# Kernel tuning notes

Hardware: AMD Instinct MI355X
Metric: run time of the kernel (lower is better)

## Reference

```python
import jax, jax.numpy as jnp
import numpy as np

NUM_GRAPHS = 128
NODES_PER_GRAPH = 512
NUM_NODES = NUM_GRAPHS * NODES_PER_GRAPH
NUM_EDGES = NUM_NODES * 16
IN_DIM = 64
HID = 128
NUM_HEADS = 4
BN_EPS = 1e-5


def setup_inputs() -> dict:
    key = jax.random.key(0)
    ks = jax.random.split(key, 12)
    x = jax.random.normal(ks[0], (NUM_NODES, IN_DIM), dtype=jnp.float32)
    edge_index = jax.random.randint(ks[1], (2, NUM_EDGES), 0, NUM_NODES, dtype=jnp.int32)
    batch = jnp.repeat(jnp.arange(NUM_GRAPHS, dtype=jnp.int32), NODES_PER_GRAPH)
    s = 0.05
    W0 = jax.random.normal(ks[2], (IN_DIM, HID), dtype=jnp.float32) * s
    b0 = jnp.zeros((HID,), jnp.float32)
    Wh = jax.random.normal(ks[3], (3, HID, HID), dtype=jnp.float32) * s  # convs 1..3
    bh = jnp.zeros((3, HID), jnp.float32)
    bn_gamma = jnp.ones((4, HID), jnp.float32)
    bn_beta = jnp.zeros((4, HID), jnp.float32)
    bn_mean = jnp.zeros((4, HID), jnp.float32)
    bn_var = jnp.ones((4, HID), jnp.float32)
    attn_in_w = jax.random.normal(ks[4], (3 * HID, HID), dtype=jnp.float32) * s
    attn_in_b = jnp.zeros((3 * HID,), jnp.float32)
    attn_out_w = jax.random.normal(ks[5], (HID, HID), dtype=jnp.float32) * s
    attn_out_b = jnp.zeros((HID,), jnp.float32)
    return dict(x=x, W0=W0, b0=b0, Wh=Wh, bh=bh, bn_gamma=bn_gamma, bn_beta=bn_beta,
                bn_mean=bn_mean, bn_var=bn_var, attn_in_w=attn_in_w, attn_in_b=attn_in_b,
                attn_out_w=attn_out_w, attn_out_b=attn_out_b, edge_index=edge_index, batch=batch)


def _forward(x, W0, b0, Wh, bh, bn_gamma, bn_beta, bn_mean, bn_var,
             attn_in_w, attn_in_b, attn_out_w, attn_out_b, edge_index, batch):
    N = x.shape[0]
    src, dst = edge_index[0], edge_index[1]
    # GCN symmetric normalization with self-loops (PyG GCNConv)
    deg = jax.ops.segment_sum(jnp.ones_like(src, jnp.float32), dst, num_segments=N) + 1.0
    dis = jax.lax.rsqrt(deg)                      # deg^{-1/2}
    enorm = (dis[src] * dis[dst])[:, None]        # per-edge norm
    self_norm = (dis * dis)[:, None]              # self-loop norm

    def gcn(h, W, b):
        h = h @ W
        agg = jax.ops.segment_sum(h[src] * enorm, dst, num_segments=N)
        return agg + h * self_norm + b

    def bn(h, i):
        scale = bn_gamma[i] * jax.lax.rsqrt(bn_var[i] + BN_EPS)
        return (h - bn_mean[i]) * scale + bn_beta[i]  # eval-mode BN

    # dropout is identity in eval mode
    h = jax.nn.relu(bn(gcn(x, W0, b0), 0))
    h = jax.nn.relu(bn(gcn(h, Wh[0], bh[0]), 1))
    h = jax.nn.relu(bn(gcn(h, Wh[1], bh[1]), 2))
    f = jax.nn.relu(bn(gcn(h, Wh[2], bh[2]), 3))   # [N, HID]

    # per-graph self-attention (equal-size contiguous graphs -> batched MHA)
    dh = HID // NUM_HEADS
    xg = f.reshape(NUM_GRAPHS, NODES_PER_GRAPH, HID)
    qkv = xg @ attn_in_w.T + attn_in_b            # [G, n, 3H]
    q, k, v = jnp.split(qkv, 3, axis=-1)

    def heads(t):
        return t.reshape(NUM_GRAPHS, NODES_PER_GRAPH, NUM_HEADS, dh).transpose(0, 2, 1, 3)
    q, k, v = heads(q), heads(k), heads(v)
    scores = jnp.einsum('ghnd,ghmd->ghnm', q, k) / np.sqrt(dh).astype(np.float32)
    attn = jax.nn.softmax(scores, axis=-1)
    o = jnp.einsum('ghnm,ghmd->ghnd', attn, v).transpose(0, 2, 1, 3).reshape(NUM_GRAPHS, NODES_PER_GRAPH, HID)
    o = o @ attn_out_w.T + attn_out_b
    final = o.reshape(N, HID)

    # global mean pool over batch indices
    cnt = jax.ops.segment_sum(jnp.ones((N,), jnp.float32), batch, num_segments=NUM_GRAPHS)
    graph_emb = jax.ops.segment_sum(final, batch, num_segments=NUM_GRAPHS) / cnt[:, None]
    return final, graph_emb


def reference(x, W0, b0, Wh, bh, bn_gamma, bn_beta, bn_mean, bn_var,
              attn_in_w, attn_in_b, attn_out_w, attn_out_b, edge_index, batch):
    return _forward(x, W0, b0, Wh, bh, bn_gamma, bn_beta, bn_mean, bn_var,
                    attn_in_w, attn_in_b, attn_out_w, attn_out_b, edge_index, batch)
```

## Files before the change

kernel.cpp:

```cpp
#include <hip/hip_runtime.h>
#include <hip/hip_bf16.h>
#include <cstdint>
#include <cstddef>

#define N_NODES 65536
#define N_EDGES 1048576
#define N_GRAPHS 128
#define NPG 512
#define IN_DIM 64
#define HID 128
#define BN_EPS 1e-5f

typedef __attribute__((ext_vector_type(8))) short bf16x8;
typedef __attribute__((ext_vector_type(4))) float f32x4;
typedef __attribute__((ext_vector_type(8))) unsigned short u16x8;

__device__ inline unsigned short f2bf(float f) {
  unsigned u = __builtin_bit_cast(unsigned, f);
  u = u + 0x7fffu + ((u >> 16) & 1u);
  return (unsigned short)(u >> 16);
}
__device__ inline float bf2f(unsigned short h) {
  unsigned u = ((unsigned)h) << 16;
  return __builtin_bit_cast(float, u);
}
__device__ inline void split_bf(float v, unsigned short& hi, unsigned short& lo) {
  hi = f2bf(v);
  lo = f2bf(v - bf2f(hi));
}

__global__ __launch_bounds__(256) void hist_kernel(const int* __restrict__ dst,
                                                   int* __restrict__ deg) {
  int e = blockIdx.x * 256 + threadIdx.x;
  if (e < N_EDGES) atomicAdd(&deg[dst[e]], 1);
}

__global__ __launch_bounds__(256) void dis_kernel(const int* __restrict__ deg,
                                                  float* __restrict__ dis) {
  int n = blockIdx.x * 256 + threadIdx.x;
  if (n < N_NODES) dis[n] = 1.0f / sqrtf((float)deg[n] + 1.0f);
}

__global__ __launch_bounds__(1024) void scan_kernel(const int* __restrict__ deg,
                                                    int* __restrict__ offsets,
                                                    int* __restrict__ cursor) {
  __shared__ int sums[1024];
  int t = threadIdx.x;
  int base = t * 64;
  const int4* dp = (const int4*)(deg + base);
  int s = 0;
#pragma unroll
  for (int i = 0; i < 16; i++) {
    int4 v = dp[i];
    s += v.x + v.y + v.z + v.w;
  }
  sums[t] = s;
  __syncthreads();
  for (int off = 1; off < 1024; off <<= 1) {
    int v = (t >= off) ? sums[t - off] : 0;
    __syncthreads();
    sums[t] += v;
    __syncthreads();
  }
  int run = (t == 0) ? 0 : sums[t - 1];
#pragma unroll
  for (int i = 0; i < 16; i++) {
    int4 v = dp[i];
    int idx = base + i * 4;
    offsets[idx] = run; cursor[idx] = run; run += v.x;
    offsets[idx + 1] = run; cursor[idx + 1] = run; run += v.y;
    offsets[idx + 2] = run; cursor[idx + 2] = run; run += v.z;
    offsets[idx + 3] = run; cursor[idx + 3] = run; run += v.w;
  }
  if (t == 1023) offsets[N_NODES] = run;
}

__global__ __launch_bounds__(256) void fill_kernel(const int* __restrict__ src,
                                                   const int* __restrict__ dst,
                                                   int* __restrict__ cursor,
                                                   int* __restrict__ csr) {
  int e = blockIdx.x * 256 + threadIdx.x;
  if (e < N_EDGES) {
    int d = dst[e];
    int slot = atomicAdd(&cursor[d], 1);
    csr[slot] = src[e];
  }
}

__global__ __launch_bounds__(256) void agg64_kernel(const float* __restrict__ x,
                                                    const float* __restrict__ dis,
                                                    const int* __restrict__ offsets,
                                                    const int* __restrict__ csr,
                                                    unsigned short* __restrict__ zhi,
                                                    unsigned short* __restrict__ zlo) {
  int node = blockIdx.x * 4 + (threadIdx.x >> 6);
  int lane = threadIdx.x & 63;
  float dn = dis[node];
  float acc = x[(size_t)node * 64 + lane] * dn * dn;
  int beg = offsets[node], end = offsets[node + 1];
  int k = beg;
  for (; k + 4 <= end; k += 4) {
    int s0 = csr[k], s1 = csr[k + 1], s2 = csr[k + 2], s3 = csr[k + 3];
    float w0 = dn * dis[s0], w1 = dn * dis[s1], w2 = dn * dis[s2], w3 = dn * dis[s3];
    float v0 = x[(size_t)s0 * 64 + lane];
    float v1 = x[(size_t)s1 * 64 + lane];
    float v2 = x[(size_t)s2 * 64 + lane];
    float v3 = x[(size_t)s3 * 64 + lane];
    acc = fmaf(w0, v0, acc);
    acc = fmaf(w1, v1, acc);
    acc = fmaf(w2, v2, acc);
    acc = fmaf(w3, v3, acc);
  }
  for (; k < end; k++) {
    int s = csr[k];
    acc = fmaf(dn * dis[s], x[(size_t)s * 64 + lane], acc);
  }
  unsigned short h_, l_;
  split_bf(acc, h_, l_);
  zhi[(size_t)node * 64 + lane] = h_;
  zlo[(size_t)node * 64 + lane] = l_;
}

__global__ __launch_bounds__(256) void agg128_kernel(const float* __restrict__ h,
                                                     const float* __restrict__ dis,
                                                     const int* __restrict__ offsets,
                                                     const int* __restrict__ csr,
                                                     unsigned short* __restrict__ zhi,
                                                     unsigned short* __restrict__ zlo) {
  int node = blockIdx.x * 4 + (threadIdx.x >> 6);
  int lane = threadIdx.x & 63;
  float dn = dis[node];
  float sn = dn * dn;
  const float* hr = h + (size_t)node * 128;
  float a0 = hr[lane] * sn;
  float a1 = hr[lane + 64] * sn;
  int beg = offsets[node], end = offsets[node + 1];
  int k = beg;
  for (; k + 4 <= end; k += 4) {
    int s0 = csr[k], s1 = csr[k + 1], s2 = csr[k + 2], s3 = csr[k + 3];
    float w0 = dn * dis[s0], w1 = dn * dis[s1], w2 = dn * dis[s2], w3 = dn * dis[s3];
    const float* p0 = h + (size_t)s0 * 128;
    const float* p1 = h + (size_t)s1 * 128;
    const float* p2 = h + (size_t)s2 * 128;
    const float* p3 = h + (size_t)s3 * 128;
    float u0 = p0[lane], d0 = p0[lane + 64];
    float u1 = p1[lane], d1 = p1[lane + 64];
    float u2 = p2[lane], d2 = p2[lane + 64];
    float u3 = p3[lane], d3 = p3[lane + 64];
    a0 = fmaf(w0, u0, a0); a1 = fmaf(w0, d0, a1);
    a0 = fmaf(w1, u1, a0); a1 = fmaf(w1, d1, a1);
    a0 = fmaf(w2, u2, a0); a1 = fmaf(w2, d2, a1);
    a0 = fmaf(w3, u3, a0); a1 = fmaf(w3, d3, a1);
  }
  for (; k < end; k++) {
    int s = csr[k];
    float w = dn * dis[s];
    const float* hs = h + (size_t)s * 128;
    a0 = fmaf(w, hs[lane], a0);
    a1 = fmaf(w, hs[lane + 64], a1);
  }
  unsigned short h0, l0, h1, l1;
  split_bf(a0, h0, l0);
  split_bf(a1, h1, l1);
  zhi[(size_t)node * 128 + lane] = h0;
  zlo[(size_t)node * 128 + lane] = l0;
  zhi[(size_t)node * 128 + lane + 64] = h1;
  zlo[(size_t)node * 128 + lane + 64] = l1;
}

template <bool TRANS>
__global__ __launch_bounds__(256) void wprep_kernel(const float* __restrict__ W, int K, int O,
                                                    unsigned short* __restrict__ hi,
                                                    unsigned short* __restrict__ lo) {
  int idx = blockIdx.x * 256 + threadIdx.x;
  int KC = K / 32;
  int total = (O / 16) * KC * 64;
  if (idx >= total) return;
  int lane = idx & 63;
  int rest = idx >> 6;
  int kc = rest % KC;
  int nt = rest / KC;
  int n = nt * 16 + (lane & 15);
  int kb = kc * 32 + (lane >> 4) * 8;
  unsigned short* hp = hi + (size_t)idx * 8;
  unsigned short* lp = lo + (size_t)idx * 8;
#pragma unroll
  for (int j = 0; j < 8; j++) {
    int k = kb + j;
    float v = TRANS ? W[(size_t)n * K + k] : W[(size_t)k * O + n];
    unsigned short h_, l_;
    split_bf(v, h_, l_);
    hp[j] = h_;
    lp[j] = l_;
  }
}

template <int K, int O, bool DOBN, bool DORELU, bool SPLIT_OUT>
__global__ __launch_bounds__(256) void gemm_mfma(
    const unsigned short* __restrict__ Ahi, const unsigned short* __restrict__ Alo,
    const unsigned short* __restrict__ Whi, const unsigned short* __restrict__ Wlo,
    const float* __restrict__ bias,
    const float* __restrict__ gamma, const float* __restrict__ beta,
    const float* __restrict__ mean, const float* __restrict__ var,
    float* __restrict__ Cf, unsigned short* __restrict__ Chi,
    unsigned short* __restrict__ Clo) {
  constexpr int KC = K / 32;
  int wave = threadIdx.x >> 6;
  int lane = threadIdx.x & 63;
  int m0 = blockIdx.x * 128 + wave * 32;
  int o0 = blockIdx.y * 128;
  int mrow = lane & 15;
  int kseg = (lane >> 4) * 8;

  f32x4 acc[2][8];
#pragma unroll
  for (int mt = 0; mt < 2; mt++)
#pragma unroll
    for (int nt = 0; nt < 8; nt++) acc[mt][nt] = (f32x4)0.0f;

#pragma unroll
  for (int kc = 0; kc < KC; kc++) {
    bf16x8 ah[2], al[2];
#pragma unroll
    for (int mt = 0; mt < 2; mt++) {
      size_t aoff = (size_t)(m0 + mt * 16 + mrow) * K + kc * 32 + kseg;
      ah[mt] = *(const bf16x8*)(Ahi + aoff);
      al[mt] = *(const bf16x8*)(Alo + aoff);
    }
#pragma unroll
    for (int nt = 0; nt < 8; nt++) {
      size_t foff = (((size_t)(blockIdx.y * 8 + nt) * KC + kc) * 64 + lane) * 8;
      bf16x8 bh = *(const bf16x8*)(Whi + foff);
      bf16x8 bl = *(const bf16x8*)(Wlo + foff);
#pragma unroll
      for (int mt = 0; mt < 2; mt++) {
        acc[mt][nt] = __builtin_amdgcn_mfma_f32_16x16x32_bf16(ah[mt], bh, acc[mt][nt], 0, 0, 0);
        acc[mt][nt] = __builtin_amdgcn_mfma_f32_16x16x32_bf16(ah[mt], bl, acc[mt][nt], 0, 0, 0);
        acc[mt][nt] = __builtin_amdgcn_mfma_f32_16x16x32_bf16(al[mt], bh, acc[mt][nt], 0, 0, 0);
        acc[mt][nt] = __builtin_amdgcn_mfma_f32_16x16x32_bf16(al[mt], bl, acc[mt][nt], 0, 0, 0);
      }
    }
  }

  int ccol = lane & 15;
  int crow0 = (lane >> 4) * 4;
#pragma unroll
  for (int nt = 0; nt < 8; nt++) {
    int c = o0 + nt * 16 + ccol;
    float sc, cb;
    float b = bias[c];
    if (DOBN) {
      sc = gamma[c] * rsqrtf(var[c] + BN_EPS);
      cb = (b - mean[c]) * sc + beta[c];
    } else {
      sc = 1.0f;
      cb = b;
    }
#pragma unroll
    for (int mt = 0; mt < 2; mt++) {
#pragma unroll
      for (int r = 0; r < 4; r++) {
        float v = fmaf(acc[mt][nt][r], sc, cb);
        if (DORELU) v = fmaxf(v, 0.0f);
        size_t row = (size_t)(m0 + mt * 16 + crow0 + r);
        if (SPLIT_OUT) {
          unsigned short h_, l_;
          split_bf(v, h_, l_);
          Chi[row * O + c] = h_;
          Clo[row * O + c] = l_;
        } else {
          Cf[row * O + c] = v;
        }
      }
    }
  }
}

__global__ __launch_bounds__(256) void knorm_kernel(const float* __restrict__ qkv,
                                                    float* __restrict__ kmax2) {
  int g = blockIdx.x >> 2;
  int h = blockIdx.x & 3;
  size_t gbase = (size_t)g * NPG;
  float best = 0.0f;
#pragma unroll
  for (int r = 0; r < 2; r++) {
    int j = r * 256 + threadIdx.x;
    const float* kp = &qkv[(gbase + j) * 384 + 128 + h * 32];
    float s = 0.0f;
#pragma unroll
    for (int i = 0; i < 8; i++) {
      float4 v = *(const float4*)(kp + i * 4);
      s = fmaf(v.x, v.x, s);
      s = fmaf(v.y, v.y, s);
      s = fmaf(v.z, v.z, s);
      s = fmaf(v.w, v.w, s);
    }
    best = fmaxf(best, s);
  }
#pragma unroll
  for (int off = 32; off >= 1; off >>= 1)
    best = fmaxf(best, __shfl_xor(best, off, 64));
  __shared__ float red[4];
  int wave = threadIdx.x >> 6;
  if ((threadIdx.x & 63) == 0) red[wave] = best;
  __syncthreads();
  if (threadIdx.x == 0) {
    float m = fmaxf(fmaxf(red[0], red[1]), fmaxf(red[2], red[3]));
    kmax2[blockIdx.x] = m;
  }
}

__global__ __launch_bounds__(256, 2) void attn_mfma_kernel(
    const float* __restrict__ qkv, const float* __restrict__ kmax2,
    unsigned short* __restrict__ ohi, unsigned short* __restrict__ olo) {
  int b = blockIdx.x;
  int g = b >> 3;
  int h = (b >> 1) & 3;
  int half = b & 1;
  int t = threadIdx.x;
  int wave = t >> 6;
  int lane = t & 63;
  int quad = lane >> 4;
  int l15 = lane & 15;
  size_t gbase = (size_t)g * NPG;
  int qb = half * 256 + wave * 64;

  const float cf = 0.17677669529663687f * 1.4426950408889634f;

  __shared__ unsigned short Kh[32][40], Kl[32][40];
  __shared__ unsigned short Vh[33][40], Vl[33][40];
  __shared__ char wbuf[4][10240] __attribute__((aligned(16)));

  unsigned short* Ph = (unsigned short*)wbuf[wave];
  unsigned short* Pl = Ph + 64 * 40;
  float* Ot = (float*)wbuf[wave];

  bf16x8 qh[4], ql[4];
  float qn2p[4];
#pragma unroll
  for (int mt = 0; mt < 4; mt++) {
    const float* qp = &qkv[(gbase + qb + mt * 16 + l15) * 384 + h * 32 + quad * 8];
    float4 f0 = *(const float4*)qp;
    float4 f1 = *(const float4*)(qp + 4);
    float v[8] = {f0.x * cf, f0.y * cf, f0.z * cf, f0.w * cf,
                  f1.x * cf, f1.y * cf, f1.z * cf, f1.w * cf};
    u16x8 hh, ll;
    float s = 0.0f;
#pragma unroll
    for (int j = 0; j < 8; j++) {
      unsigned short hi_, lo_;
      split_bf(v[j], hi_, lo_);
      hh[j] = hi_;
      ll[j] = lo_;
      s = fmaf(v[j], v[j], s);
    }
    qh[mt] = __builtin_bit_cast(bf16x8, hh);
    ql[mt] = __builtin_bit_cast(bf16x8, ll);
    s += __shfl_xor(s, 16);
    s += __shfl_xor(s, 32);
    qn2p[mt] = s;
  }
  if (quad == 0) {
#pragma unroll
    for (int mt = 0; mt < 4; mt++) Ot[mt * 16 + l15] = qn2p[mt];
  }
  float km2 = kmax2[g * 4 + h];
  float Mq[4][4];
#pragma unroll
  for (int mt = 0; mt < 4; mt++)
#pragma unroll
    for (int r = 0; r < 4; r++)
      Mq[mt][r] = sqrtf(Ot[mt * 16 + quad * 4 + r] * km2);

  f32x4 Oa[4][3];
#pragma unroll
  for (int mt = 0; mt < 4; mt++)
#pragma unroll
    for (int nt = 0; nt < 3; nt++) Oa[mt][nt] = (f32x4)0.0f;

  for (int c = 0; c < 16; c++) {
    __syncthreads();
    if (t >= 128) {
      int t2 = t - 128;
      int key = t2 >> 2;
      int ds = (t2 & 3) * 8;
      const float* kp = &qkv[(gbase + (size_t)(c * 32 + key)) * 384 + 128 + h * 32 + ds];
      float4 f0 = *(const float4*)kp;
      float4 f1 = *(const float4*)(kp + 4);
      float v[8] = {f0.x, f0.y, f0.z, f0.w, f1.x, f1.y, f1.z, f1.w};
      u16x8 hh, ll;
#pragma unroll
      for (int j = 0; j < 8; j++) {
        unsigned short hi_, lo_;
        split_bf(v[j], hi_, lo_);
        hh[j] = hi_;
        ll[j] = lo_;
      }
      *(u16x8*)&Kh[key][ds] = hh;
      *(u16x8*)&Kl[key][ds] = ll;
    } else if (t < 64) {
      int keyb = (t & 7) * 4;
      int dvb = (t >> 3) * 4;
      float4 r0 = *(const float4*)&qkv[(gbase + (size_t)(c * 32 + keyb + 0)) * 384 + 256 + h * 32 + dvb];
      float4 r1 = *(const float4*)&qkv[(gbase + (size_t)(c * 32 + keyb + 1)) * 384 + 256 + h * 32 + dvb];
      float4 r2 = *(const float4*)&qkv[(gbase + (size_t)(c * 32 + keyb + 2)) * 384 + 256 + h * 32 + dvb];
      float4 r3 = *(const float4*)&qkv[(gbase + (size_t)(c * 32 + keyb + 3)) * 384 + 256 + h * 32 + dvb];
      float rr[4][4] = {{r0.x, r0.y, r0.z, r0.w}, {r1.x, r1.y, r1.z, r1.w},
                        {r2.x, r2.y, r2.z, r2.w}, {r3.x, r3.y, r3.z, r3.w}};
#pragma unroll
      for (int c2 = 0; c2 < 4; c2++) {
        ushort4 hv, lv;
        unsigned short hi_, lo_;
        split_bf(rr[0][c2], hi_, lo_); hv.x = hi_; lv.x = lo_;
        split_bf(rr[1][c2], hi_, lo_); hv.y = hi_; lv.y = lo_;
        split_bf(rr[2][c2], hi_, lo_); hv.z = hi_; lv.z = lo_;
        split_bf(rr[3][c2], hi_, lo_); hv.w = hi_; lv.w = lo_;
        *(ushort4*)&Vh[dvb + c2][keyb] = hv;
        *(ushort4*)&Vl[dvb + c2][keyb] = lv;
      }
    } else if (t < 68) {
      int i = t - 64;
      u16x8 ones;
#pragma unroll
      for (int j = 0; j < 8; j++) ones[j] = 0x3F80;
      *(u16x8*)&Vh[32][i * 8] = ones;
    }
    __syncthreads();

#pragma unroll
    for (int nt = 0; nt < 2; nt++) {
      bf16x8 bkh = *(const bf16x8*)&Kh[nt * 16 + l15][quad * 8];
      bf16x8 bkl = *(const bf16x8*)&Kl[nt * 16 + l15][quad * 8];
#pragma unroll
      for (int mt = 0; mt < 4; mt++) {
        f32x4 S = (f32x4)0.0f;
        S = __builtin_amdgcn_mfma_f32_16x16x32_bf16(qh[mt], bkh, S, 0, 0, 0);
        S = __builtin_amdgcn_mfma_f32_16x16x32_bf16(qh[mt], bkl, S, 0, 0, 0);
        S = __builtin_amdgcn_mfma_f32_16x16x32_bf16(ql[mt], bkh, S, 0, 0, 0);
        S = __builtin_amdgcn_mfma_f32_16x16x32_bf16(ql[mt], bkl, S, 0, 0, 0);
#pragma unroll
        for (int r = 0; r < 4; r++) {
          float p = __builtin_exp2f(S[r] - Mq[mt][r]);
          unsigned short hi_, lo_;
          split_bf(p, hi_, lo_);
          int row = mt * 16 + quad * 4 + r;
          Ph[row * 40 + nt * 16 + l15] = hi_;
          Pl[row * 40 + nt * 16 + l15] = lo_;
        }
      }
    }
    bf16x8 pah[4], pal[4];
#pragma unroll
    for (int mt = 0; mt < 4; mt++) {
      pah[mt] = *(const bf16x8*)&Ph[(mt * 16 + l15) * 40 + quad * 8];
      pal[mt] = *(const bf16x8*)&Pl[(mt * 16 + l15) * 40 + quad * 8];
    }
#pragma unroll
    for (int nt = 0; nt < 3; nt++) {
      bf16x8 bvh = *(const bf16x8*)&Vh[nt * 16 + l15][quad * 8];
      if (nt < 2) {
        bf16x8 bvl = *(const bf16x8*)&Vl[nt * 16 + l15][quad * 8];
#pragma unroll
        for (int mt = 0; mt < 4; mt++) {
          Oa[mt][nt] = __builtin_amdgcn_mfma_f32_16x16x32_bf16(pah[mt], bvh, Oa[mt][nt], 0, 0, 0);
          Oa[mt][nt] = __builtin_amdgcn_mfma_f32_16x16x32_bf16(pah[mt], bvl, Oa[mt][nt], 0, 0, 0);
          Oa[mt][nt] = __builtin_amdgcn_mfma_f32_16x16x32_bf16(pal[mt], bvh, Oa[mt][nt], 0, 0, 0);
        }
      } else {
#pragma unroll
        for (int mt = 0; mt < 4; mt++) {
          Oa[mt][nt] = __builtin_amdgcn_mfma_f32_16x16x32_bf16(pah[mt], bvh, Oa[mt][nt], 0, 0, 0);
          Oa[mt][nt] = __builtin_amdgcn_mfma_f32_16x16x32_bf16(pal[mt], bvh, Oa[mt][nt], 0, 0, 0);
        }
      }
    }
  }

#pragma unroll
  for (int mt = 0; mt < 4; mt++) {
#pragma unroll
    for (int r = 0; r < 4; r++) {
      int row = mt * 16 + quad * 4 + r;
      Ot[row * 36 + l15] = Oa[mt][0][r];
      Ot[row * 36 + 16 + l15] = Oa[mt][1][r];
      if (l15 == 0) Ot[row * 36 + 32] = Oa[mt][2][r];
    }
  }
  {
    int row = lane;
    float inv = 1.0f / Ot[row * 36 + 32];
    size_t node = gbase + qb + row;
    u16x8 vh, vl;
#pragma unroll
    for (int seg = 0; seg < 4; seg++) {
#pragma unroll
      for (int j = 0; j < 8; j++) {
        unsigned short hi_, lo_;
        split_bf(Ot[row * 36 + seg * 8 + j] * inv, hi_, lo_);
        vh[j] = hi_;
        vl[j] = lo_;
      }
      *(u16x8*)(ohi + node * 128 + h * 32 + seg * 8) = vh;
      *(u16x8*)(olo + node * 128 + h * 32 + seg * 8) = vl;
    }
  }
}

__global__ __launch_bounds__(128) void pool_kernel(const float* __restrict__ fin,
                                                   float* __restrict__ emb) {
  int g = blockIdx.x, c = threadIdx.x;
  const float* p = fin + (size_t)g * NPG * HID + c;
  float s = 0.0f;
  for (int i = 0; i < NPG; i++) s += p[(size_t)i * HID];
  emb[g * HID + c] = s * (1.0f / NPG);
}

extern "C" void kernel_launch(void* const* d_in, const int* in_sizes, int n_in,
                              void* d_out, int out_size, void* d_ws, size_t ws_size,
                              hipStream_t stream) {
  (void)in_sizes; (void)n_in; (void)out_size; (void)ws_size;
  const float* x          = (const float*)d_in[0];
  const float* W0         = (const float*)d_in[1];
  const float* b0         = (const float*)d_in[2];
  const float* Wh         = (const float*)d_in[3];
  const float* bh         = (const float*)d_in[4];
  const float* bn_gamma   = (const float*)d_in[5];
  const float* bn_beta    = (const float*)d_in[6];
  const float* bn_mean    = (const float*)d_in[7];
  const float* bn_var     = (const float*)d_in[8];
  const float* attn_in_w  = (const float*)d_in[9];
  const float* attn_in_b  = (const float*)d_in[10];
  const float* attn_out_w = (const float*)d_in[11];
  const float* attn_out_b = (const float*)d_in[12];
  const int* edge_index   = (const int*)d_in[13];
  const int* src = edge_index;
  const int* dst = edge_index + N_EDGES;

  char* ws = (char*)d_ws;
  size_t off = 0;
  auto alloc = [&](size_t bytes) -> void* {
    void* p = ws + off;
    off += (bytes + 255) & ~(size_t)255;
    return p;
  };
  int*   deg     = (int*)alloc((size_t)N_NODES * 4);
  int*   offsets = (int*)alloc((size_t)(N_NODES + 1) * 4);
  int*   cursor  = (int*)alloc((size_t)N_NODES * 4);
  int*   csr     = (int*)alloc((size_t)N_EDGES * 4);
  float* dis     = (float*)alloc((size_t)N_NODES * 4);
  float* bufA    = (float*)alloc((size_t)N_NODES * HID * 4);
  unsigned short* zhi = (unsigned short*)alloc((size_t)N_NODES * HID * 2);
  unsigned short* zlo = (unsigned short*)alloc((size_t)N_NODES * HID * 2);
  float* qkvb    = (float*)alloc((size_t)N_NODES * 384 * 4);
  float* kmax2   = (float*)alloc((size_t)N_GRAPHS * 4 * 4);
  unsigned short* w0h = (unsigned short*)alloc(8192 * 2);
  unsigned short* w0l = (unsigned short*)alloc(8192 * 2);
  unsigned short* whh[3], *whl[3];
  for (int i = 0; i < 3; i++) {
    whh[i] = (unsigned short*)alloc(16384 * 2);
    whl[i] = (unsigned short*)alloc(16384 * 2);
  }
  unsigned short* wqh = (unsigned short*)alloc(49152 * 2);
  unsigned short* wql = (unsigned short*)alloc(49152 * 2);
  unsigned short* woh = (unsigned short*)alloc(16384 * 2);
  unsigned short* wol = (unsigned short*)alloc(16384 * 2);

  unsigned short* fhi = (unsigned short*)bufA;
  unsigned short* flo = fhi + (size_t)N_NODES * HID;

  float* fin = (float*)d_out;
  float* emb = fin + (size_t)N_NODES * HID;

  hipMemsetAsync(deg, 0, (size_t)N_NODES * 4, stream);
  hist_kernel<<<N_EDGES / 256, 256, 0, stream>>>(dst, deg);
  dis_kernel<<<N_NODES / 256, 256, 0, stream>>>(deg, dis);
  scan_kernel<<<1, 1024, 0, stream>>>(deg, offsets, cursor);
  fill_kernel<<<N_EDGES / 256, 256, 0, stream>>>(src, dst, cursor, csr);

  wprep_kernel<false><<<4, 256, 0, stream>>>(W0, 64, 128, w0h, w0l);
  for (int i = 0; i < 3; i++)
    wprep_kernel<false><<<8, 256, 0, stream>>>(Wh + (size_t)i * HID * HID, 128, 128,
                                               whh[i], whl[i]);
  wprep_kernel<true><<<24, 256, 0, stream>>>(attn_in_w, 128, 384, wqh, wql);
  wprep_kernel<true><<<8, 256, 0, stream>>>(attn_out_w, 128, 128, woh, wol);

  dim3 ggrid(N_NODES / 128, 1);
  agg64_kernel<<<N_NODES / 4, 256, 0, stream>>>(x, dis, offsets, csr, zhi, zlo);
  gemm_mfma<64, 128, true, true, false><<<ggrid, 256, 0, stream>>>(
      zhi, zlo, w0h, w0l, b0, bn_gamma, bn_beta, bn_mean, bn_var, bufA, nullptr, nullptr);
  for (int L = 0; L < 2; L++) {
    agg128_kernel<<<N_NODES / 4, 256, 0, stream>>>(bufA, dis, offsets, csr, zhi, zlo);
    gemm_mfma<128, 128, true, true, false><<<ggrid, 256, 0, stream>>>(
        zhi, zlo, whh[L], whl[L], bh + (size_t)L * HID,
        bn_gamma + (size_t)(L + 1) * HID, bn_beta + (size_t)(L + 1) * HID,
        bn_mean + (size_t)(L + 1) * HID, bn_var + (size_t)(L + 1) * HID,
        bufA, nullptr, nullptr);
  }
  agg128_kernel<<<N_NODES / 4, 256, 0, stream>>>(bufA, dis, offsets, csr, zhi, zlo);
  gemm_mfma<128, 128, true, true, true><<<ggrid, 256, 0, stream>>>(
      zhi, zlo, whh[2], whl[2], bh + (size_t)2 * HID,
      bn_gamma + (size_t)3 * HID, bn_beta + (size_t)3 * HID,
      bn_mean + (size_t)3 * HID, bn_var + (size_t)3 * HID,
      nullptr, fhi, flo);
  dim3 qgrid(N_NODES / 128, 3);
  gemm_mfma<128, 384, false, false, false><<<qgrid, 256, 0, stream>>>(
      fhi, flo, wqh, wql, attn_in_b, nullptr, nullptr, nullptr, nullptr,
      qkvb, nullptr, nullptr);
  knorm_kernel<<<N_GRAPHS * 4, 256, 0, stream>>>(qkvb, kmax2);
  attn_mfma_kernel<<<N_GRAPHS * 4 * 2, 256, 0, stream>>>(qkvb, kmax2, zhi, zlo);
  gemm_mfma<128, 128, false, false, false><<<ggrid, 256, 0, stream>>>(
      zhi, zlo, woh, wol, attn_out_b, nullptr, nullptr, nullptr, nullptr,
      fin, nullptr, nullptr);
  pool_kernel<<<N_GRAPHS, 128, 0, stream>>>(fin, emb);
}
```

Before: 851.0 us.

## Emit QKV as split bf16 hi/lo from GEMM and drop re-splitting in attention

The QKV projection GEMM now writes bf16 hi/lo pairs directly instead of fp32, so the attention and knorm kernels load pre-split operands rather than converting fp32 on every K/V chunk load. The softmax scale is folded into the exponent via an fma, and a cheaper truncating hi/lo split is used for probabilities and outputs. The pool kernel is split four ways per graph with atomic accumulation into a zeroed buffer. This changes rounding slightly (truncated hi for P and outputs, q not pre-scaled before splitting) and adds an extra memset plus atomics.

```diff
diff --git a/kernel.cpp b/kernel.cpp
--- a/kernel.cpp
+++ b/kernel.cpp
@@ -27,6 +27,12 @@
 __device__ inline void split_bf(float v, unsigned short& hi, unsigned short& lo) {
   hi = f2bf(v);
   lo = f2bf(v - bf2f(hi));
+}
+__device__ inline void split_bf_fast(float v, unsigned short& hi, unsigned short& lo) {
+  unsigned u = __builtin_bit_cast(unsigned, v);
+  hi = (unsigned short)(u >> 16);
+  float r = v - __builtin_bit_cast(float, u & 0xffff0000u);
+  lo = f2bf(r);
 }
 
 __global__ __launch_bounds__(256) void hist_kernel(const int* __restrict__ dst,
@@ -276,7 +282,8 @@
   }
 }
 
-__global__ __launch_bounds__(256) void knorm_kernel(const float* __restrict__ qkv,
+__global__ __launch_bounds__(256) void knorm_kernel(const unsigned short* __restrict__ qh_,
+                                                    const unsigned short* __restrict__ ql_,
                                                     float* __restrict__ kmax2) {
   int g = blockIdx.x >> 2;
   int h = blockIdx.x & 3;
@@ -285,15 +292,17 @@
 #pragma unroll
   for (int r = 0; r < 2; r++) {
     int j = r * 256 + threadIdx.x;
-    const float* kp = &qkv[(gbase + j) * 384 + 128 + h * 32];
+    size_t base = (gbase + j) * 384 + 128 + (size_t)h * 32;
     float s = 0.0f;
 #pragma unroll
-    for (int i = 0; i < 8; i++) {
-      float4 v = *(const float4*)(kp + i * 4);
-      s = fmaf(v.x, v.x, s);
-      s = fmaf(v.y, v.y, s);
-      s = fmaf(v.z, v.z, s);
-      s = fmaf(v.w, v.w, s);
+    for (int i = 0; i < 4; i++) {
+      u16x8 hh = *(const u16x8*)(qh_ + base + i * 8);
+      u16x8 ll = *(const u16x8*)(ql_ + base + i * 8);
+#pragma unroll
+      for (int jj = 0; jj < 8; jj++) {
+        float v = bf2f(hh[jj]) + bf2f(ll[jj]);
+        s = fmaf(v, v, s);
+      }
     }
     best = fmaxf(best, s);
   }
@@ -311,7 +320,8 @@
 }
 
 __global__ __launch_bounds__(256, 2) void attn_mfma_kernel(
-    const float* __restrict__ qkv, const float* __restrict__ kmax2,
+    const unsigned short* __restrict__ qh_, const unsigned short* __restrict__ ql_,
+    const float* __restrict__ kmax2,
     unsigned short* __restrict__ ohi, unsigned short* __restrict__ olo) {
   int b = blockIdx.x;
   int g = b >> 3;
@@ -339,23 +349,17 @@
   float qn2p[4];
 #pragma unroll
   for (int mt = 0; mt < 4; mt++) {
-    const float* qp = &qkv[(gbase + qb + mt * 16 + l15) * 384 + h * 32 + quad * 8];
-    float4 f0 = *(const float4*)qp;
-    float4 f1 = *(const float4*)(qp + 4);
-    float v[8] = {f0.x * cf, f0.y * cf, f0.z * cf, f0.w * cf,
-                  f1.x * cf, f1.y * cf, f1.z * cf, f1.w * cf};
-    u16x8 hh, ll;
-    float s = 0.0f;
-#pragma unroll
-    for (int j = 0; j < 8; j++) {
-      unsigned short hi_, lo_;
-      split_bf(v[j], hi_, lo_);
-      hh[j] = hi_;
-      ll[j] = lo_;
-      s = fmaf(v[j], v[j], s);
-    }
+    size_t qoff = (gbase + qb + mt * 16 + l15) * 384 + (size_t)h * 32 + quad * 8;
+    u16x8 hh = *(const u16x8*)(qh_ + qoff);
+    u16x8 ll = *(const u16x8*)(ql_ + qoff);
     qh[mt] = __builtin_bit_cast(bf16x8, hh);
     ql[mt] = __builtin_bit_cast(bf16x8, ll);
+    float s = 0.0f;
+#pragma unroll
+    for (int j = 0; j < 8; j++) {
+      float v = bf2f(hh[j]) + bf2f(ll[j]);
+      s = fmaf(v, v, s);
+    }
     s += __shfl_xor(s, 16);
     s += __shfl_xor(s, 32);
     qn2p[mt] = s;
@@ -370,7 +374,7 @@
   for (int mt = 0; mt < 4; mt++)
 #pragma unroll
     for (int r = 0; r < 4; r++)
-      Mq[mt][r] = sqrtf(Ot[mt * 16 + quad * 4 + r] * km2);
+      Mq[mt][r] = cf * sqrtf(Ot[mt * 16 + quad * 4 + r] * km2);
 
   f32x4 Oa[4][3];
 #pragma unroll
@@ -384,37 +388,24 @@
       int t2 = t - 128;
       int key = t2 >> 2;
       int ds = (t2 & 3) * 8;
-      const float* kp = &qkv[(gbase + (size_t)(c * 32 + key)) * 384 + 128 + h * 32 + ds];
-      float4 f0 = *(const float4*)kp;
-      float4 f1 = *(const float4*)(kp + 4);
-      float v[8] = {f0.x, f0.y, f0.z, f0.w, f1.x, f1.y, f1.z, f1.w};
-      u16x8 hh, ll;
-#pragma unroll
-      for (int j = 0; j < 8; j++) {
-        unsigned short hi_, lo_;
-        split_bf(v[j], hi_, lo_);
-        hh[j] = hi_;
-        ll[j] = lo_;
-      }
-      *(u16x8*)&Kh[key][ds] = hh;
-      *(u16x8*)&Kl[key][ds] = ll;
+      size_t ko = (gbase + (size_t)(c * 32 + key)) * 384 + 128 + (size_t)h * 32 + ds;
+      *(u16x8*)&Kh[key][ds] = *(const u16x8*)(qh_ + ko);
+      *(u16x8*)&Kl[key][ds] = *(const u16x8*)(ql_ + ko);
     } else if (t < 64) {
       int keyb = (t & 7) * 4;
       int dvb = (t >> 3) * 4;
-      float4 r0 = *(const float4*)&qkv[(gbase + (size_t)(c * 32 + keyb + 0)) * 384 + 256 + h * 32 + dvb];
-      float4 r1 = *(const float4*)&qkv[(gbase + (size_t)(c * 32 + keyb + 1)) * 384 + 256 + h * 32 + dvb];
-      float4 r2 = *(const float4*)&qkv[(gbase + (size_t)(c * 32 + keyb + 2)) * 384 + 256 + h * 32 + dvb];
-      float4 r3 = *(const float4*)&qkv[(gbase + (size_t)(c * 32 + keyb + 3)) * 384 + 256 + h * 32 + dvb];
-      float rr[4][4] = {{r0.x, r0.y, r0.z, r0.w}, {r1.x, r1.y, r1.z, r1.w},
-                        {r2.x, r2.y, r2.z, r2.w}, {r3.x, r3.y, r3.z, r3.w}};
+      unsigned short ha[4][4], la[4][4];
+#pragma unroll
+      for (int r = 0; r < 4; r++) {
+        size_t vo = (gbase + (size_t)(c * 32 + keyb + r)) * 384 + 256 + (size_t)h * 32 + dvb;
+        *(ushort4*)&ha[r][0] = *(const ushort4*)(qh_ + vo);
+        *(ushort4*)&la[r][0] = *(const ushort4*)(ql_ + vo);
+      }
 #pragma unroll
       for (int c2 = 0; c2 < 4; c2++) {
         ushort4 hv, lv;
-        unsigned short hi_, lo_;
-        split_bf(rr[0][c2], hi_, lo_); hv.x = hi_; lv.x = lo_;
-        split_bf(rr[1][c2], hi_, lo_); hv.y = hi_; lv.y = lo_;
-        split_bf(rr[2][c2], hi_, lo_); hv.z = hi_; lv.z = lo_;
-        split_bf(rr[3][c2], hi_, lo_); hv.w = hi_; lv.w = lo_;
+        hv.x = ha[0][c2]; hv.y = ha[1][c2]; hv.z = ha[2][c2]; hv.w = ha[3][c2];
+        lv.x = la[0][c2]; lv.y = la[1][c2]; lv.z = la[2][c2]; lv.w = la[3][c2];
         *(ushort4*)&Vh[dvb + c2][keyb] = hv;
         *(ushort4*)&Vl[dvb + c2][keyb] = lv;
       }
@@ -440,9 +431,9 @@
         S = __builtin_amdgcn_mfma_f32_16x16x32_bf16(ql[mt], bkl, S, 0, 0, 0);
 #pragma unroll
         for (int r = 0; r < 4; r++) {
-          float p = __builtin_exp2f(S[r] - Mq[mt][r]);
+          float p = __builtin_exp2f(fmaf(S[r], cf, -Mq[mt][r]));
           unsigned short hi_, lo_;
-          split_bf(p, hi_, lo_);
+          split_bf_fast(p, hi_, lo_);
           int row = mt * 16 + quad * 4 + r;
           Ph[row * 40 + nt * 16 + l15] = hi_;
           Pl[row * 40 + nt * 16 + l15] = lo_;
@@ -496,7 +487,7 @@
 #pragma unroll
       for (int j = 0; j < 8; j++) {
         unsigned short hi_, lo_;
-        split_bf(Ot[row * 36 + seg * 8 + j] * inv, hi_, lo_);
+        split_bf_fast(Ot[row * 36 + seg * 8 + j] * inv, hi_, lo_);
         vh[j] = hi_;
         vl[j] = lo_;
       }
@@ -508,11 +499,14 @@
 
 __global__ __launch_bounds__(128) void pool_kernel(const float* __restrict__ fin,
                                                    float* __restrict__ emb) {
-  int g = blockIdx.x, c = threadIdx.x;
-  const float* p = fin + (size_t)g * NPG * HID + c;
+  int g = blockIdx.x >> 2;
+  int q = blockIdx.x & 3;
+  int c = threadIdx.x;
+  const float* p = fin + ((size_t)g * NPG + (size_t)q * 128) * HID + c;
   float s = 0.0f;
-  for (int i = 0; i < NPG; i++) s += p[(size_t)i * HID];
-  emb[g * HID + c] = s * (1.0f / NPG);
+#pragma unroll 4
+  for (int i = 0; i < 128; i++) s += p[(size_t)i * HID];
+  atomicAdd(&emb[g * HID + c], s * (1.0f / NPG));
 }
 
 extern "C" void kernel_launch(void* const* d_in, const int* in_sizes, int n_in,
@@ -551,7 +545,8 @@
   float* bufA    = (float*)alloc((size_t)N_NODES * HID * 4);
   unsigned short* zhi = (unsigned short*)alloc((size_t)N_NODES * HID * 2);
   unsigned short* zlo = (unsigned short*)alloc((size_t)N_NODES * HID * 2);
-  float* qkvb    = (float*)alloc((size_t)N_NODES * 384 * 4);
+  unsigned short* qvh = (unsigned short*)alloc((size_t)N_NODES * 384 * 2);
+  unsigned short* qvl = (unsigned short*)alloc((size_t)N_NODES * 384 * 2);
   float* kmax2   = (float*)alloc((size_t)N_GRAPHS * 4 * 4);
   unsigned short* w0h = (unsigned short*)alloc(8192 * 2);
   unsigned short* w0l = (unsigned short*)alloc(8192 * 2);
@@ -572,6 +567,7 @@
   float* emb = fin + (size_t)N_NODES * HID;
 
   hipMemsetAsync(deg, 0, (size_t)N_NODES * 4, stream);
+  hipMemsetAsync(emb, 0, (size_t)N_GRAPHS * HID * 4, stream);
   hist_kernel<<<N_EDGES / 256, 256, 0, stream>>>(dst, deg);
   dis_kernel<<<N_NODES / 256, 256, 0, stream>>>(deg, dis);
   scan_kernel<<<1, 1024, 0, stream>>>(deg, offsets, cursor);
@@ -603,13 +599,13 @@
       bn_mean + (size_t)3 * HID, bn_var + (size_t)3 * HID,
       nullptr, fhi, flo);
   dim3 qgrid(N_NODES / 128, 3);
-  gemm_mfma<128, 384, false, false, false><<<qgrid, 256, 0, stream>>>(
+  gemm_mfma<128, 384, false, false, true><<<qgrid, 256, 0, stream>>>(
       fhi, flo, wqh, wql, attn_in_b, nullptr, nullptr, nullptr, nullptr,
-      qkvb, nullptr, nullptr);
-  knorm_kernel<<<N_GRAPHS * 4, 256, 0, stream>>>(qkvb, kmax2);
-  attn_mfma_kernel<<<N_GRAPHS * 4 * 2, 256, 0, stream>>>(qkvb, kmax2, zhi, zlo);
+      nullptr, qvh, qvl);
+  knorm_kernel<<<N_GRAPHS * 4, 256, 0, stream>>>(qvh, qvl, kmax2);
+  attn_mfma_kernel<<<N_GRAPHS * 4 * 2, 256, 0, stream>>>(qvh, qvl, kmax2, zhi, zlo);
   gemm_mfma<128, 128, false, false, false><<<ggrid, 256, 0, stream>>>(
       zhi, zlo, woh, wol, attn_out_b, nullptr, nullptr, nullptr, nullptr,
       fin, nullptr, nullptr);
-  pool_kernel<<<N_GRAPHS, 128, 0, stream>>>(fin, emb);
-}
+  pool_kernel<<<N_GRAPHS * 4, 128, 0, stream>>>(fin, emb);
+}
```

After: 849.7 us. No clear change (-0.1%).
